# Optimization experiments

Measured on AMD Instinct MI355X. Metric: run time of the kernel, lower is better.

The kernel has to match this reference:

```python
import jax, jax.numpy as jnp
import numpy as np

PATCH = 3
STRIDE = 1

def _extract_patches(style, k, s):
    # style: [C,H,W] -> patches [n2*n3, C, k, k], matching torch unfold(1).unfold(2).permute(1,2,0,3,4)
    C, H, W = style.shape
    n2 = (H - k) // s + 1
    n3 = (W - k) // s + 1
    ih = (jnp.arange(n2) * s)[:, None] + jnp.arange(k)[None, :]   # [n2,k]
    iw = (jnp.arange(n3) * s)[:, None] + jnp.arange(k)[None, :]   # [n3,k]
    p = style[:, ih, :]                 # [C,n2,k,W]
    p = p[:, :, :, iw]                  # [C,n2,k,n3,k]
    p = jnp.transpose(p, (1, 3, 0, 2, 4))  # [n2,n3,C,k,k]
    return p.reshape(n2 * n3, C, k, k)

def _conv_transpose_nchw(x, w_io, s, k):
    # torch ConvTranspose2d with weight [in_ch,out_ch,k,k], stride s, padding 0
    w = jnp.transpose(jnp.flip(w_io, axis=(2, 3)), (1, 0, 2, 3))  # OIHW, O=out_ch
    return jax.lax.conv_general_dilated(
        x, w, window_strides=(1, 1), padding=[(k - 1, k - 1), (k - 1, k - 1)],
        lhs_dilation=(s, s), dimension_numbers=('NCHW', 'OIHW', 'NCHW'))

def setup_inputs() -> dict:
    key = jax.random.key(0)
    k0, k1, k2, k3, k4 = jax.random.split(key, 5)
    B, C, H, W = 4, 256, 64, 64
    n = (H - PATCH) // STRIDE + 1
    npatches = n * n  # 3844
    return {
        'content':    jax.random.normal(k0, (B, C, H, W), dtype=jnp.float32),
        'style_img':  jax.random.normal(k1, (C, H, W), dtype=jnp.float32),
        'enc_bias':   jax.random.normal(k2, (npatches,), dtype=jnp.float32) * 0.01,
        'dec_bias':   jax.random.normal(k3, (C,), dtype=jnp.float32) * 0.01,
        'intra_bias': jax.random.normal(k4, (C,), dtype=jnp.float32) * 0.01,
    }

def reference(content, style_img, enc_bias, dec_bias, intra_bias):
    patches = _extract_patches(style_img, PATCH, STRIDE)  # [np, C, k, k]
    npatches = patches.shape[0]
    # conv_enc: cross-correlate content with style patches (note: the torch code's
    # patch normalization uses non-inplace .mul, so it is a no-op -> raw patches)
    feat = jax.lax.conv_general_dilated(
        content, patches, (STRIDE, STRIDE), 'VALID',
        dimension_numbers=('NCHW', 'OIHW', 'NCHW')) + enc_bias[None, :, None, None]
    # maxCoord: top-1 one-hot over the patch (channel) axis, no gradient
    idx = jnp.argmax(feat, axis=1)                                     # [B,H',W']
    onehot = jnp.moveaxis(jax.nn.one_hot(idx, npatches, dtype=feat.dtype), -1, 1)
    onehot = jax.lax.stop_gradient(onehot)                             # [B,np,H',W']
    # conv_dec: transposed conv with style patches (overlap-add of selected patch)
    dec = _conv_transpose_nchw(onehot, patches, STRIDE, PATCH) + dec_bias[None, :, None, None]
    # conv_intra: transposed conv with all-ones kernel -> overlap counts
    ones_w = jnp.ones_like(patches)
    intra = _conv_transpose_nchw(onehot, ones_w, STRIDE, PATCH) + intra_bias[None, :, None, None]
    return dec / intra
```

## Files before the change

kernel.cpp:

```cpp
#include <hip/hip_runtime.h>
#include <stdint.h>

#define NP   3844
#define ND   62
#define NC   256
#define HW   64
#define SP   4096
#define SPSP ((size_t)SP * SP)
#define NCSP ((size_t)NC * SP)
#define EPS_G 0.15f
#define HULP_H 0.0009765625f
#define SPLIT_REL 0.0009765625f

#define EP_ROWS 65
#define EP_LD   132

typedef __attribute__((ext_vector_type(8))) short short8;
typedef __attribute__((ext_vector_type(8))) unsigned short ushort8;
typedef __attribute__((ext_vector_type(8))) _Float16 half8;
typedef __attribute__((ext_vector_type(2))) _Float16 half2v;
typedef __attribute__((ext_vector_type(4))) float float4v;
typedef __attribute__((ext_vector_type(2))) float float2v;
typedef unsigned long long u64;

__device__ __forceinline__ unsigned int orderf(float v) {
    unsigned int u = __float_as_uint(v);
    return (u & 0x80000000u) ? ~u : (u | 0x80000000u);
}
__device__ __forceinline__ float unorderf(unsigned int k) {
    return __uint_as_float((k & 0x80000000u) ? (k ^ 0x80000000u) : ~k);
}

__device__ __forceinline__ int xcd_swz(int orig, int nwg) {
    const int q = nwg >> 3, r = nwg & 7;
    const int xcd = orig & 7, i = orig >> 3;
    const int base = (xcd < r) ? xcd * (q + 1) : r * (q + 1) + (xcd - r) * q;
    return base + i;
}

__global__ __launch_bounds__(256) void transpose_b(
    const float* __restrict__ src0, float* __restrict__ dst0)
{
    const float* src = src0 + (size_t)blockIdx.z * NCSP;
    float* dst = dst0 + (size_t)blockIdx.z * NCSP;
    __shared__ float t[32][33];
    const int s0 = blockIdx.x * 32;
    const int c0 = blockIdx.y * 32;
    const int col = threadIdx.x & 31, r8 = threadIdx.x >> 5;
    #pragma unroll
    for (int i = 0; i < 4; ++i) {
        int r = r8 + i * 8;
        t[r][col] = src[(size_t)(c0 + r) * SP + s0 + col];
    }
    __syncthreads();
    #pragma unroll
    for (int i = 0; i < 4; ++i) {
        int r = r8 + i * 8;
        dst[(size_t)(s0 + r) * 256 + c0 + col] = t[col][r];
    }
}

__global__ __launch_bounds__(256) void col_sq(
    const float* __restrict__ content, const float* __restrict__ style,
    float* __restrict__ na_c, float* __restrict__ nb_s)
{
    const int blk = blockIdx.x, tid = threadIdx.x, qn = blockIdx.y;
    const float* src;
    float* dst;
    int s;
    if (blk < 64) {
        int b = blk >> 4, ch = blk & 15;
        src = content + (size_t)b * NCSP;
        dst = na_c + b * SP;
        s = ch * 256 + tid;
    } else {
        src = style;
        dst = nb_s;
        s = (blk - 64) * 256 + tid;
    }
    float sum = 0.f;
    const int c0 = qn * 64;
    #pragma unroll 4
    for (int c = c0; c < c0 + 64; ++c) {
        float v = src[(size_t)c * SP + s];
        sum = fmaf(v, v, sum);
    }
    atomicAdd(&dst[s], sum);
}

__global__ __launch_bounds__(256) void panels_f16(
    const float* __restrict__ src0, unsigned short* __restrict__ P0)
{
    const float* src = src0 + (size_t)blockIdx.z * NCSP;
    unsigned short* P = P0 + (size_t)blockIdx.z * NCSP;

    __shared__ unsigned short buf[512 * 8];
    const int kp = blockIdx.x;
    const int s0 = blockIdx.y * 512;
    const int tid = threadIdx.x;
    #pragma unroll
    for (int kk = 0; kk < 8; ++kk) {
        #pragma unroll
        for (int h = 0; h < 2; ++h) {
            int s = tid + h * 256;
            float a = src[(size_t)(kp * 8 + kk) * SP + s0 + s];
            _Float16 hf = (_Float16)a;
            unsigned short hb;
            __builtin_memcpy(&hb, &hf, 2);
            buf[s * 8 + kk] = hb;
        }
    }
    __syncthreads();
    #pragma unroll
    for (int h = 0; h < 2; ++h) {
        int s = tid + h * 256;
        size_t o = ((size_t)kp * 4096 + s0 + s) * 8;
        *(ushort8*)(P + o) = *(const ushort8*)(buf + s * 8);
    }
}

__device__ __forceinline__ void epilogue_H(
    float* __restrict__ Lt, const float4v acc[4][4],
    int tid, int wm, int wn, int fq, int fr,
    unsigned short* __restrict__ Hb, int s0, int t0)
{
    #pragma unroll
    for (int p = 0; p < 2; ++p) {
        const int rb = p * 63;
        __syncthreads();
        #pragma unroll
        for (int fm = 0; fm < 4; ++fm) {
            #pragma unroll
            for (int r = 0; r < 4; ++r) {
                const int row = wm + fm * 16 + fq * 4 + r;
                const int lr = row - rb;
                if (lr >= 0 && lr < EP_ROWS) {
                    #pragma unroll
                    for (int fn = 0; fn < 4; ++fn)
                        Lt[lr * EP_LD + wn + fn * 16 + fr] = acc[fm][fn][r];
                }
            }
        }
        __syncthreads();

        for (int task = tid; task < 63 * 16; task += 256) {
            const int rl = task >> 4;
            const int rr = rb + rl;
            const int o  = (task & 15) * 8;
            const float* L0 = Lt + rl * EP_LD + o;
            const float* L1 = L0 + EP_LD;
            const float* L2 = L0 + 2 * EP_LD;
            float4v r0a = *(const float4v*)(L0);
            float4v r0b = *(const float4v*)(L0 + 4);
            float4v r1a = *(const float4v*)(L1);
            float4v r1b = *(const float4v*)(L1 + 4);
            float2v r1c = *(const float2v*)(L1 + 8);
            float4v r2a = *(const float4v*)(L2);
            float4v r2b = *(const float4v*)(L2 + 4);
            float2v r2c = *(const float2v*)(L2 + 8);
            float s_[8];
            s_[0] = r0a[0] + r1a[1] + r2a[2];
            s_[1] = r0a[1] + r1a[2] + r2a[3];
            s_[2] = r0a[2] + r1a[3] + r2b[0];
            s_[3] = r0a[3] + r1b[0] + r2b[1];
            s_[4] = r0b[0] + r1b[1] + r2b[2];
            s_[5] = r0b[1] + r1b[2] + r2b[3];
            s_[6] = r0b[2] + r1b[3] + r2c[0];
            s_[7] = r0b[3] + r1c[0] + r2c[1];
            unsigned short* hp = Hb + (size_t)(s0 + rr) * SP + t0 + o;
            const int kmax = (o == 120) ? 3 : 4;
            #pragma unroll
            for (int k = 0; k < 4; ++k) {
                if (k < kmax) {
                    half2v hv;
                    hv[0] = (_Float16)s_[2 * k];
                    hv[1] = (_Float16)s_[2 * k + 1];
                    *(half2v*)(hp + 2 * k) = hv;
                }
            }
        }
    }
}

__global__ __launch_bounds__(256) void g_gemm_f16(
    const unsigned short* __restrict__ A0,
    const unsigned short* __restrict__ B,
    unsigned short* __restrict__ H0)
{
    __shared__ __attribute__((aligned(16))) float Lt[EP_ROWS * EP_LD];

    const int orig = blockIdx.x + 33 * blockIdx.y + 1089 * blockIdx.z;
    const int wg = xcd_swz(orig, 4356);
    const int bz = wg / 1089;
    const int rem = wg - bz * 1089;
    const int by = rem / 33;
    const int bx = rem - by * 33;

    const unsigned short* A = A0 + (size_t)bz * NCSP;
    unsigned short* Hb = H0 + (size_t)bz * SPSP;

    const int tid  = threadIdx.x;
    const int s0   = (bx < 32) ? bx * 126 : 3968;
    const int t0   = (by < 32) ? by * 126 : 3968;
    const int wave = tid >> 6, lane = tid & 63;
    const int wm = (wave >> 1) * 64, wn = (wave & 1) * 64;
    const int fr = lane & 15;
    const int fq = lane >> 4;

    float4v acc[4][4];
    #pragma unroll
    for (int i = 0; i < 4; ++i)
        #pragma unroll
        for (int j = 0; j < 4; ++j) acc[i][j] = (float4v)(0.f);

    size_t ra0[4], rb0[4];
    #pragma unroll
    for (int f = 0; f < 4; ++f) {
        ra0[f] = ((size_t)fq * 4096 + s0 + wm + f * 16 + fr) * 8;
        rb0[f] = ((size_t)fq * 4096 + t0 + wn + f * 16 + fr) * 8;
    }

    #pragma unroll 4
    for (int ks = 0; ks < 8; ++ks) {
        const size_t pan = (size_t)ks * 4 * 4096 * 8;
        half8 a[4], b[4];
        #pragma unroll
        for (int f = 0; f < 4; ++f) {
            a[f] = *(const half8*)(A + pan + ra0[f]);
            b[f] = *(const half8*)(B + pan + rb0[f]);
        }
        #pragma unroll
        for (int fm = 0; fm < 4; ++fm)
            #pragma unroll
            for (int fn = 0; fn < 4; ++fn)
                acc[fm][fn] = __builtin_amdgcn_mfma_f32_16x16x32_f16(
                    a[fm], b[fn], acc[fm][fn], 0, 0, 0);
    }

    epilogue_H(Lt, acc, tid, wm, wn, fq, fr, Hb, s0, t0);
}

__global__ __launch_bounds__(256, 2) void g_gemm(
    const float* __restrict__ contentb,
    const float* __restrict__ style,
    unsigned short* __restrict__ Hb)
{
    __shared__ __attribute__((aligned(16))) char smem[65536];
    short* Ah = (short*)smem;
    short* Al = Ah + 4096;
    short* Bh = Al + 4096;
    short* Bl = Bh + 4096;

    const int orig = blockIdx.x + 33 * blockIdx.y;
    const int wg = xcd_swz(orig, 1089);
    const int by = wg / 33;
    const int bx = wg - by * 33;

    const int tid  = threadIdx.x;
    const int s0   = (bx < 32) ? bx * 126 : 3968;
    const int t0   = (by < 32) ? by * 126 : 3968;
    const int wave = tid >> 6, lane = tid & 63;
    const int wm = (wave >> 1) * 64, wn = (wave & 1) * 64;
    const int fr = lane & 15;
    const int fq = lane >> 4;
    const int sm = tid & 127;
    const int sl = tid >> 7;

    float4v acc[4][4];
    #pragma unroll
    for (int i = 0; i < 4; ++i)
        #pragma unroll
        for (int j = 0; j < 4; ++j) acc[i][j] = (float4v)(0.f);

    for (int k0 = 0; k0 < 256; k0 += 32) {
        __syncthreads();
        #pragma unroll
        for (int h = 0; h < 2; ++h) {
            const float* src = h ? style : contentb;
            const int rb = h ? t0 : s0;
            short* dh = h ? Bh : Ah;
            short* dl = h ? Bl : Al;
            float v[16];
            #pragma unroll
            for (int j = 0; j < 16; ++j)
                v[j] = src[(size_t)(k0 + sl * 16 + j) * SP + rb + sm];
            short8 h0, h1, l0, l1;
            #pragma unroll
            for (int j = 0; j < 8; ++j) {
                unsigned ua = __float_as_uint(v[j]);
                unsigned ub = __float_as_uint(v[j + 8]);
                h0[j] = (short)(ua >> 16);
                h1[j] = (short)(ub >> 16);
                float ra  = v[j]     - __uint_as_float(ua & 0xffff0000u);
                float rb2 = v[j + 8] - __uint_as_float(ub & 0xffff0000u);
                l0[j] = (short)(__float_as_uint(ra) >> 16);
                l1[j] = (short)(__float_as_uint(rb2) >> 16);
            }
            *(short8*)(dh + ((sl * 2)     * 128 + sm) * 8) = h0;
            *(short8*)(dh + ((sl * 2 + 1) * 128 + sm) * 8) = h1;
            *(short8*)(dl + ((sl * 2)     * 128 + sm) * 8) = l0;
            *(short8*)(dl + ((sl * 2 + 1) * 128 + sm) * 8) = l1;
        }
        __syncthreads();

        short8 ah[4], al[4], bh[4], bl[4];
        #pragma unroll
        for (int f = 0; f < 4; ++f) {
            const int ra = (fq * 128 + wm + f * 16 + fr) * 8;
            const int rb = (fq * 128 + wn + f * 16 + fr) * 8;
            ah[f] = *(const short8*)(Ah + ra);
            al[f] = *(const short8*)(Al + ra);
            bh[f] = *(const short8*)(Bh + rb);
            bl[f] = *(const short8*)(Bl + rb);
        }
        #pragma unroll
        for (int fm = 0; fm < 4; ++fm)
            #pragma unroll
            for (int fn = 0; fn < 4; ++fn) {
                acc[fm][fn] = __builtin_amdgcn_mfma_f32_16x16x32_bf16(ah[fm], bh[fn], acc[fm][fn], 0, 0, 0);
                acc[fm][fn] = __builtin_amdgcn_mfma_f32_16x16x32_bf16(ah[fm], bl[fn], acc[fm][fn], 0, 0, 0);
                acc[fm][fn] = __builtin_amdgcn_mfma_f32_16x16x32_bf16(al[fm], bh[fn], acc[fm][fn], 0, 0, 0);
            }
    }

    epilogue_H((float*)smem, acc, tid, wm, wn, fq, fr, Hb, s0, t0);
}

__global__ __launch_bounds__(256) void stencil_h(
    const unsigned short* __restrict__ H0,
    const float* __restrict__ enc_bias,
    u64* __restrict__ cand2, int bbase)
{
    const int bl = blockIdx.y;
    const unsigned short* H = H0 + (size_t)bl * SPSP;
    const int b = bbase + bl;

    const int q = blockIdx.x * 4 + (threadIdx.x >> 6);
    const int lane = threadIdx.x & 63;
    const int y = q / ND, x = q - y * ND;
    const int jg = (lane & 7) * 8;
    const int ig = lane >> 3;
    const unsigned short* Hq0 = H + (size_t)(y * 64 + x) * SP;
    const unsigned short* Hq1 = Hq0 + (size_t)64 * SP;
    const unsigned short* Hq2 = Hq0 + (size_t)128 * SP;

    float fb1[4], fb2[4];
    int   ib1[4], ib2[4];
    #pragma unroll
    for (int s = 0; s < 4; ++s) {
        fb1[s] = -3.0e38f; fb2[s] = -3.0e38f; ib1[s] = 0; ib2[s] = 0;
    }

    for (int it = 0; it < 8; ++it) {
        const int i = it * 8 + ig;
        if (i <= 61) {
            const int t0o = i * 64 + jg;
            half8 w0 = *(const half8*)(Hq0 + t0o);
            half8 w1 = *(const half8*)(Hq1 + t0o + 64);
            half8 w2 = *(const half8*)(Hq2 + t0o + 128);
            const float* ep = enc_bias + i * ND + jg;
            float eb[8];
            {
                float2v a0 = *(const float2v*)(ep);
                float2v a1 = *(const float2v*)(ep + 2);
                float2v a2 = *(const float2v*)(ep + 4);
                eb[0] = a0[0]; eb[1] = a0[1];
                eb[2] = a1[0]; eb[3] = a1[1];
                eb[4] = a2[0]; eb[5] = a2[1];
                if (jg < 56) {
                    float2v a3 = *(const float2v*)(ep + 6);
                    eb[6] = a3[0]; eb[7] = a3[1];
                } else { eb[6] = 0.f; eb[7] = 0.f; }
            }
            const int pq = i * ND + jg;
            #pragma unroll
            for (int j = 0; j < 8; ++j) {
                int jj = jg + j;
                if (jj <= 61) {
                    float fv = ((float)w0[j] + (float)w1[j])
                             + ((float)w2[j] + eb[j]);
                    int p = pq + j;
                    const int s = j >> 1;
                    bool gt1 = fv > fb1[s];
                    bool gt2 = fv > fb2[s];
                    fb2[s] = gt1 ? fb1[s] : (gt2 ? fv : fb2[s]);
                    ib2[s] = gt1 ? ib1[s] : (gt2 ? p  : ib2[s]);
                    fb1[s] = gt1 ? fv : fb1[s];
                    ib1[s] = gt1 ? p  : ib1[s];
                }
            }
        }
    }

    u64 k1 = 0, k2 = 0;
    #pragma unroll
    for (int s = 0; s < 4; ++s) {
        u64 ka = ((u64)orderf(fb1[s]) << 32) | (unsigned)(NP - 1 - ib1[s]);
        u64 kb = ((u64)orderf(fb2[s]) << 32) | (unsigned)(NP - 1 - ib2[s]);
        if (ka > k1) { k2 = k1; k1 = ka; } else if (ka > k2) k2 = ka;
        if (kb > k1) { k2 = k1; k1 = kb; } else if (kb > k2) k2 = kb;
    }

    #pragma unroll
    for (int d = 1; d < 64; d <<= 1) {
        u64 o1 = __shfl_xor(k1, d, 64);
        u64 o2 = __shfl_xor(k2, d, 64);
        u64 hi = k1 > o1 ? k1 : o1;
        u64 lo = k1 > o1 ? o1 : k1;
        u64 m2 = k2 > o2 ? k2 : o2;
        k1 = hi;
        k2 = lo > m2 ? lo : m2;
    }
    if (lane == 0) {
        size_t o = (size_t)(b * NP + q) * 2;
        cand2[o] = k1;
        cand2[o + 1] = k2;
    }
}

__global__ __launch_bounds__(128) void rescore6(
    const float* __restrict__ content_t,
    const float* __restrict__ style_t,
    const float* __restrict__ enc_bias,
    const unsigned short* __restrict__ H0,
    const float* __restrict__ na_c,
    const float* __restrict__ nb_s,
    const u64* __restrict__ cand2,
    int* __restrict__ idx, int bbase)
{
    __shared__ float sc[2];
    __shared__ int   pp[2];
    const int bl = blockIdx.x / NP;
    const int q  = blockIdx.x - bl * NP;
    const int b  = bbase + bl;
    const int qa = b * NP + q;
    const unsigned short* Hx = H0 + (size_t)bl * SPSP;
    const int tid = threadIdx.x;
    const int wave = tid >> 6, lane = tid & 63;
    const int y = q / ND, x = q - y * ND;

    const u64 k1 = cand2[(size_t)qa * 2];
    const u64 k2 = cand2[(size_t)qa * 2 + 1];
    const int p1 = NP - 1 - (int)(k1 & 0xffffffffu);
    const int p2 = NP - 1 - (int)(k2 & 0xffffffffu);
    const float f1 = unorderf((unsigned int)(k1 >> 32));
    const float f2 = unorderf((unsigned int)(k2 >> 32));

    if (k2 == 0ull) {
        if (tid == 0) idx[qa] = p1;
        return;
    }

    float eul = 0.f;
    {
        const int side = lane >> 4;
        const int d = lane & 15;
        if (side < 2 && d < 9) {
            int u = d / 3, v = d - u * 3;
            int pc = side ? p2 : p1;
            int pi = pc / ND, pj = pc - pi * ND;
            int sd = (y + u) * 64 + (x + v);
            int td = (pi + u) * 64 + (pj + v);
            float t = SPLIT_REL * sqrtf(na_c[b * SP + sd] * nb_s[td]);
            if (v == 0) {
                unsigned short hh = Hx[(size_t)sd * SP + td];
                float hf = (float)(*(const _Float16*)&hh);
                t += __uint_as_float(__float_as_uint(hf) & 0x7f800000u) * HULP_H;
            }
            eul = t;
        }
    }
    #pragma unroll
    for (int d = 1; d < 64; d <<= 1) eul += __shfl_xor(eul, d, 64);

    if ((f1 - f2) > eul + EPS_G) {
        if (tid == 0) idx[qa] = p1;
        return;
    }

    const int pc = wave ? p2 : p1;
    const int pi = pc / ND, pj = pc - pi * ND;
    const float* ctb = content_t + (size_t)b * NCSP;
    float s = 0.f;
    #pragma unroll
    for (int u = 0; u < 3; ++u) {
        #pragma unroll
        for (int v = 0; v < 3; ++v) {
            const float* cw = ctb + (size_t)((y + u) * 64 + x + v) * 256 + lane * 4;
            const float* sw = style_t + (size_t)((pi + u) * 64 + pj + v) * 256 + lane * 4;
            float4v c4 = *(const float4v*)cw;
            float4v s4 = *(const float4v*)sw;
            s = fmaf(c4[0], s4[0], s);
            s = fmaf(c4[1], s4[1], s);
            s = fmaf(c4[2], s4[2], s);
            s = fmaf(c4[3], s4[3], s);
        }
    }
    #pragma unroll
    for (int d = 32; d; d >>= 1) s += __shfl_xor(s, d, 64);
    if (lane == 0) { sc[wave] = s + enc_bias[pc]; pp[wave] = pc; }
    __syncthreads();
    if (tid == 0) {
        float s0 = sc[0], s1 = sc[1];
        int q0 = pp[0], q1 = pp[1];
        idx[qa] = (s1 > s0 || (s1 == s0 && q1 < q0)) ? q1 : q0;
    }
}

__global__ __launch_bounds__(256) void produce_out2(
    const float* __restrict__ style_t,
    const float* __restrict__ dec_bias,
    const float* __restrict__ intra_bias,
    const int* __restrict__ idx,
    float* __restrict__ out)
{
    __shared__ float orow[64][129];
    __shared__ int pidx[3][ND];

    const int bh = blockIdx.x;
    const int b = bh >> 6, h = bh & 63;
    const int ch = blockIdx.y;
    const int tid = threadIdx.x;

    if (tid < 3 * ND) {
        int u = tid / ND, xx = tid - u * ND;
        int yy = h - u;
        pidx[u][xx] = (yy >= 0 && yy < ND) ? idx[b * NP + yy * ND + xx] : 0;
    }
    for (int i = tid; i < 64 * 129; i += 256) ((float*)orow)[i] = 0.f;
    __syncthreads();

    const int cl = tid & 127;
    const int xo = tid >> 7;
    for (int u = 0; u < 3; ++u) {
        int yy = h - u;
        if (yy < 0 || yy >= ND) continue;
        #pragma unroll
        for (int v = 0; v < 3; ++v) {
            for (int xi = (xo + v) & 1; xi < ND; xi += 2) {
                int p = pidx[u][xi];
                int pi = p / ND, pj = p - pi * ND;
                float sv = style_t[(size_t)(pi * 64 + pj + u * 64 + v) * 256 + ch * 128 + cl];
                orow[xi + v][cl] += sv;
            }
        }
    }
    __syncthreads();

    const int w = tid & 63, cg = tid >> 6;
    const int cu  = (h < 2 ? h : 2) - (h > 61 ? h - 61 : 0) + 1;
    const int cvw = (w < 2 ? w : 2) - (w > 61 ? w - 61 : 0) + 1;
    const float cnt = (float)(cu * cvw);
    #pragma unroll 4
    for (int ci = 0; ci < 32; ++ci) {
        int cll = cg * 32 + ci;
        int c = ch * 128 + cll;
        float val = (orow[w][cll] + dec_bias[c]) / (cnt + intra_bias[c]);
        out[(((size_t)b * NC + c) * 64 + h) * 64 + w] = val;
    }
}

extern "C" void kernel_launch(void* const* d_in, const int* in_sizes, int n_in,
                              void* d_out, int out_size, void* d_ws, size_t ws_size,
                              hipStream_t stream) {
    const float* content    = (const float*)d_in[0];
    const float* style      = (const float*)d_in[1];
    const float* enc_bias   = (const float*)d_in[2];
    const float* dec_bias   = (const float*)d_in[3];
    const float* intra_bias = (const float*)d_in[4];
    float* out = (float*)d_out;

    const size_t H_BYTES     = SPSP * 2;
    const size_t CAND2_BYTES = (size_t)4 * NP * 2 * 8;
    const size_t IDX_BYTES   = (size_t)4 * NP * 4;
    const size_t ST_BYTES    = NCSP * 4;
    const size_t CT_BYTES    = (size_t)4 * NCSP * 4;
    const size_t P16_BYTES   = NCSP * 2;
    const size_t NA_BYTES    = (size_t)4 * SP * 4;
    const size_t NB_BYTES    = (size_t)SP * 4;

    const size_t A_OFF_CAND2 = 4 * H_BYTES;
    const size_t A_OFF_IDX   = A_OFF_CAND2 + CAND2_BYTES;
    const size_t A_OFF_ST    = A_OFF_IDX + IDX_BYTES;
    const size_t A_OFF_CT    = A_OFF_ST + ST_BYTES;
    const size_t A_OFF_PS    = A_OFF_CT + CT_BYTES;
    const size_t A_OFF_PC    = A_OFF_PS + P16_BYTES;
    const size_t A_OFF_NA    = A_OFF_PC + 4 * P16_BYTES;
    const size_t A_OFF_NB    = A_OFF_NA + NA_BYTES;
    const size_t NEED_A      = A_OFF_NB + NB_BYTES;

    const size_t B_OFF_CAND2 = H_BYTES;
    const size_t B_OFF_IDX   = B_OFF_CAND2 + CAND2_BYTES;
    const size_t B_OFF_ST    = B_OFF_IDX + IDX_BYTES;
    const size_t B_OFF_CT    = B_OFF_ST + ST_BYTES;
    const size_t B_OFF_NA    = B_OFF_CT + CT_BYTES;
    const size_t B_OFF_NB    = B_OFF_NA + NA_BYTES;
    const size_t NEED_B      = B_OFF_NB + NB_BYTES;
    (void)NEED_B;

    if (ws_size >= NEED_A) {
        unsigned short* H4 = (unsigned short*)d_ws;
        u64* cand2      = (u64*)((char*)d_ws + A_OFF_CAND2);
        int* idx        = (int*)((char*)d_ws + A_OFF_IDX);
        float* style_t  = (float*)((char*)d_ws + A_OFF_ST);
        float* content_t = (float*)((char*)d_ws + A_OFF_CT);
        unsigned short* PS = (unsigned short*)((char*)d_ws + A_OFF_PS);
        unsigned short* PC = (unsigned short*)((char*)d_ws + A_OFF_PC);
        float* na_c     = (float*)((char*)d_ws + A_OFF_NA);
        float* nb_s     = (float*)((char*)d_ws + A_OFF_NB);

        hipMemsetAsync((char*)d_ws + A_OFF_NA, 0, NA_BYTES + NB_BYTES, stream);
        transpose_b<<<dim3(128, 8, 1), 256, 0, stream>>>(style, style_t);
        transpose_b<<<dim3(128, 8, 4), 256, 0, stream>>>(content, content_t);
        col_sq<<<dim3(80, 4), 256, 0, stream>>>(content, style, na_c, nb_s);
        panels_f16<<<dim3(32, 8, 1), 256, 0, stream>>>(style, PS);
        panels_f16<<<dim3(32, 8, 4), 256, 0, stream>>>(content, PC);
        g_gemm_f16<<<dim3(33, 33, 4), 256, 0, stream>>>(PC, PS, H4);
        stencil_h<<<dim3(NP / 4, 4), 256, 0, stream>>>(H4, enc_bias, cand2, 0);
        rescore6<<<dim3(4 * NP), 128, 0, stream>>>(
            content_t, style_t, enc_bias, H4, na_c, nb_s, cand2, idx, 0);
        produce_out2<<<dim3(4 * 64, 2), 256, 0, stream>>>(
            style_t, dec_bias, intra_bias, idx, out);
    } else {
        unsigned short* Hb = (unsigned short*)d_ws;
        u64* cand2      = (u64*)((char*)d_ws + B_OFF_CAND2);
        int* idx        = (int*)((char*)d_ws + B_OFF_IDX);
        float* style_t  = (float*)((char*)d_ws + B_OFF_ST);
        float* content_t = (float*)((char*)d_ws + B_OFF_CT);
        float* na_c     = (float*)((char*)d_ws + B_OFF_NA);
        float* nb_s     = (float*)((char*)d_ws + B_OFF_NB);

        hipMemsetAsync((char*)d_ws + B_OFF_NA, 0, NA_BYTES + NB_BYTES, stream);
        transpose_b<<<dim3(128, 8, 1), 256, 0, stream>>>(style, style_t);
        transpose_b<<<dim3(128, 8, 4), 256, 0, stream>>>(content, content_t);
        col_sq<<<dim3(80, 4), 256, 0, stream>>>(content, style, na_c, nb_s);
        for (int b = 0; b < 4; ++b) {
            g_gemm<<<dim3(33, 33), 256, 0, stream>>>(
                content + (size_t)b * NCSP, style, Hb);
            stencil_h<<<dim3(NP / 4, 1), 256, 0, stream>>>(Hb, enc_bias, cand2, b);
            rescore6<<<dim3(NP), 128, 0, stream>>>(
                content_t, style_t, enc_bias, Hb, na_c, nb_s, cand2, idx, b);
        }
        produce_out2<<<dim3(4 * 64, 2), 256, 0, stream>>>(
            style_t, dec_bias, intra_bias, idx, out);
    }
}
```

Before: 250.1 us.

## Double-buffer g_gemm_f16 operand tiles in LDS via direct global-to-LDS loads

The f16 GEMM kernel used to load each wave's A/B fragments straight from global memory into registers. It now stages each 4-k-plane panel for the whole workgroup into LDS with global_load_lds, double-buffered so the next panel loads while MFMAs run on the current one, then reads fragments from LDS. This lets waves share loads and overlaps memory with compute. In exchange it adds a __syncthreads per k-step and reuses the epilogue's LDS buffer for staging.

After: 256.0 us. +2.3%, slower.

```diff
diff --git a/kernel.cpp b/kernel.cpp
--- a/kernel.cpp
+++ b/kernel.cpp
@@ -29,6 +29,12 @@
 }
 __device__ __forceinline__ float unorderf(unsigned int k) {
     return __uint_as_float((k & 0x80000000u) ? (k ^ 0x80000000u) : ~k);
+}
+
+__device__ __forceinline__ void gload_lds16(const void* g, void* l) {
+    __builtin_amdgcn_global_load_lds(
+        (const __attribute__((address_space(1))) unsigned int*)g,
+        (__attribute__((address_space(3))) unsigned int*)l, 16, 0, 0);
 }
 
 __device__ __forceinline__ int xcd_swz(int orig, int nwg) {
@@ -187,7 +193,7 @@
     const unsigned short* __restrict__ B,
     unsigned short* __restrict__ H0)
 {
-    __shared__ __attribute__((aligned(16))) float Lt[EP_ROWS * EP_LD];
+    __shared__ __attribute__((aligned(16))) char smem[EP_ROWS * EP_LD * 4];
 
     const int orig = blockIdx.x + 33 * blockIdx.y + 1089 * blockIdx.z;
     const int wg = xcd_swz(orig, 4356);
@@ -213,21 +219,34 @@
         #pragma unroll
         for (int j = 0; j < 4; ++j) acc[i][j] = (float4v)(0.f);
 
-    size_t ra0[4], rb0[4];
-    #pragma unroll
-    for (int f = 0; f < 4; ++f) {
-        ra0[f] = ((size_t)fq * 4096 + s0 + wm + f * 16 + fr) * 8;
-        rb0[f] = ((size_t)fq * 4096 + t0 + wn + f * 16 + fr) * 8;
-    }
-
-    #pragma unroll 4
+    auto stage = [&](int ks, int bf) {
+        char* base = smem + bf * 16384;
+        #pragma unroll
+        for (int h = 0; h < 2; ++h) {
+            const int e   = h * 256 + wave * 64;
+            const int kpl = e >> 7;
+            const int sb  = e & 127;
+            const size_t ko = (size_t)(ks * 4 + kpl) * 4096;
+            gload_lds16(A + (ko + s0 + sb + lane) * 8, base + e * 16);
+            gload_lds16(B + (ko + t0 + sb + lane) * 8, base + 8192 + e * 16);
+        }
+    };
+
+    stage(0, 0);
+    __syncthreads();
+
+    #pragma unroll
     for (int ks = 0; ks < 8; ++ks) {
-        const size_t pan = (size_t)ks * 4 * 4096 * 8;
+        const int cur = ks & 1;
+        if (ks < 7) stage(ks + 1, cur ^ 1);
+
+        const char* bA = smem + cur * 16384;
+        const char* bB = bA + 8192;
         half8 a[4], b[4];
         #pragma unroll
         for (int f = 0; f < 4; ++f) {
-            a[f] = *(const half8*)(A + pan + ra0[f]);
-            b[f] = *(const half8*)(B + pan + rb0[f]);
+            a[f] = *(const half8*)(bA + (fq * 128 + wm + f * 16 + fr) * 16);
+            b[f] = *(const half8*)(bB + (fq * 128 + wn + f * 16 + fr) * 16);
         }
         #pragma unroll
         for (int fm = 0; fm < 4; ++fm)
@@ -235,9 +254,10 @@
             for (int fn = 0; fn < 4; ++fn)
                 acc[fm][fn] = __builtin_amdgcn_mfma_f32_16x16x32_f16(
                     a[fm], b[fn], acc[fm][fn], 0, 0, 0);
-    }
-
-    epilogue_H(Lt, acc, tid, wm, wn, fq, fr, Hb, s0, t0);
+        __syncthreads();
+    }
+
+    epilogue_H((float*)smem, acc, tid, wm, wn, fq, fr, Hb, s0, t0);
 }
 
 __global__ __launch_bounds__(256, 2) void g_gemm(
```
